# Optimization experiments

Measured on AMD Instinct MI355X. Metric: run time of the kernel, lower is better.

## Reference

```python
import jax, jax.numpy as jnp
import numpy as np

N_NODES = 100000
IN_CH = 256
OUT_CH = 64
N_EDGES = 3200000


def setup_inputs() -> dict:
    key = jax.random.key(0)
    k1, k2, k3, k4 = jax.random.split(key, 4)
    x = jax.random.normal(k1, (N_NODES, IN_CH), dtype=jnp.float32)
    edge_index = jax.random.randint(k2, (2, N_EDGES), 0, N_NODES, dtype=jnp.int64)
    # GCNConv parameters (glorot-style init for W, zeros for bias as in PyG)
    W = jax.random.normal(k3, (IN_CH, OUT_CH), dtype=jnp.float32) / np.sqrt(IN_CH)
    b = jnp.zeros((OUT_CH,), dtype=jnp.float32)
    return {"x": x, "edge_index": edge_index, "W": W, "b": b}


def reference(x, edge_index, W, b):
    N = x.shape[0]
    # --- GCNConv: add self-loops, symmetric degree normalization ---
    loops = jnp.arange(N, dtype=edge_index.dtype)
    src = jnp.concatenate([edge_index[0], loops])  # [E+N]
    dst = jnp.concatenate([edge_index[1], loops])  # [E+N]
    # degree of each target node (edge weights = 1)
    deg = jax.ops.segment_sum(jnp.ones_like(dst, dtype=x.dtype), dst, num_segments=N)
    dinv = jnp.where(deg > 0, jax.lax.rsqrt(deg), 0.0)  # deg^{-1/2}
    norm = dinv[src] * dinv[dst]                        # [E+N]
    # linear transform first (PyG applies lin before propagate)
    h = x @ W                                           # [N, OUT_CH]
    msg = h[src] * norm[:, None]                        # gather + scale
    out = jax.ops.segment_sum(msg, dst, num_segments=N) + b  # scatter-add + bias
    # --- relu + log_softmax ---
    out = jax.nn.relu(out)
    return jax.nn.log_softmax(out, axis=-1)
```

## Files before the change

### kernel.cpp

```cpp
#include <hip/hip_runtime.h>
#include <cstddef>
#include <cstdint>

#define N_NODES 100000
#define IN_CH 256
#define OUT_CH 64
#define N_EDGES 3200000

#define BKT_SHIFT 7
#define BKT_R     128
#define K_BKT     782
#define BKT_CAP   6144
#define T_PART    8192
#define NBLK_PART ((N_EDGES + T_PART - 1) / T_PART)
#define NBLK_GEMM 512
#define N_TILES   (N_NODES / 16)

#define WS_FLAG_OFF   0
#define WS_GCNT_OFF   64
#define WS_DINV_OFF   4096
#define WS_NSE_OFF    404096
#define WS_EDG_OFF    1204224
#define WS_H_OFF      20422656
#define WS_NEED       33222656

#define WSF_DEG_OFF   4096
#define WSF_DINV_OFF  404096
#define WSF_H_OFF     804096

typedef __attribute__((ext_vector_type(8))) short bshort8;
typedef __attribute__((ext_vector_type(4))) float f32x4;
typedef __attribute__((ext_vector_type(2))) float f32x2;
typedef __attribute__((ext_vector_type(4))) unsigned u32x4;

static __device__ __forceinline__ unsigned short f2bf(float f) {
    unsigned u = __builtin_bit_cast(unsigned, f);
    u += 0x7FFFu + ((u >> 16) & 1u);
    return (unsigned short)(u >> 16);
}
static __device__ __forceinline__ float bflo(unsigned u) {
    return __builtin_bit_cast(float, u << 16);
}
static __device__ __forceinline__ float bfhi(unsigned u) {
    return __builtin_bit_cast(float, u & 0xFFFF0000u);
}
static __device__ __forceinline__ f32x2 up2(unsigned u) {
    f32x2 r;
    r.x = __builtin_bit_cast(float, u << 16);
    r.y = __builtin_bit_cast(float, u & 0xFFFF0000u);
    return r;
}

__global__ void probe_kernel(const unsigned* __restrict__ ei, int* __restrict__ flag,
                             unsigned* __restrict__ gcnt) {
    if (blockIdx.x == 0) {
        for (int k = threadIdx.x; k < K_BKT; k += 64) gcnt[k] = 0u;
        if (threadIdx.x == 0) {
            int all0 = 1;
            for (int i = 0; i < 16; ++i) all0 &= (ei[2 * i + 1] == 0u);
            *flag = all0;
        }
    }
}

__device__ __forceinline__ int load_idx(const int* ei32, const long long* ei64,
                                        bool is64, long long pos) {
    return is64 ? (int)ei64[pos] : ei32[pos];
}

static __device__ __forceinline__ void gemm_body(char* smem, int gbid, int nblk,
                                                 const float* __restrict__ x,
                                                 const float* __restrict__ W,
                                                 unsigned short* __restrict__ hs) {
    unsigned short (*Wf)[4][64][8] = (unsigned short (*)[4][64][8])smem;
    const int tid = threadIdx.x;
    const int lane = tid & 63;
    const int wv = tid >> 6;

    for (int i = tid; i < 8 * 4 * 64 * 8; i += 256) {
        int kt = i >> 11;
        int rem = i & 2047;
        int ct = rem >> 9;
        int rem2 = rem & 511;
        int l = rem2 >> 3;
        int j = rem2 & 7;
        int kk = kt * 32 + (l >> 4) * 8 + j;
        int cc = ct * 16 + (l & 15);
        ((unsigned short*)Wf)[i] = f2bf(W[(size_t)kk * OUT_CH + cc]);
    }
    __syncthreads();

    const int r16 = lane & 15;
    const int q = lane >> 4;

    for (int t = gbid * 4 + wv; t < N_TILES; t += nblk * 4) {
        const int row0 = t * 16;
        const float* xrow = &x[(size_t)(row0 + r16) * IN_CH + q * 8];
        f32x4 acc[4] = {{0.f,0.f,0.f,0.f},{0.f,0.f,0.f,0.f},
                        {0.f,0.f,0.f,0.f},{0.f,0.f,0.f,0.f}};
        #pragma unroll
        for (int kt = 0; kt < 8; ++kt) {
            float4 x0 = *(const float4*)&xrow[kt * 32];
            float4 x1 = *(const float4*)&xrow[kt * 32 + 4];
            unsigned p0, p1, p2, p3;
            asm("v_cvt_pk_bf16_f32 %0, %1, %2" : "=v"(p0) : "v"(x0.x), "v"(x0.y));
            asm("v_cvt_pk_bf16_f32 %0, %1, %2" : "=v"(p1) : "v"(x0.z), "v"(x0.w));
            asm("v_cvt_pk_bf16_f32 %0, %1, %2" : "=v"(p2) : "v"(x1.x), "v"(x1.y));
            asm("v_cvt_pk_bf16_f32 %0, %1, %2" : "=v"(p3) : "v"(x1.z), "v"(x1.w));
            u32x4 au = {p0, p1, p2, p3};
            bshort8 af = __builtin_bit_cast(bshort8, au);
            #pragma unroll
            for (int ct = 0; ct < 4; ++ct) {
                bshort8 bf = *(const bshort8*)&Wf[kt][ct][lane][0];
                acc[ct] = __builtin_amdgcn_mfma_f32_16x16x32_bf16(af, bf, acc[ct], 0, 0, 0);
            }
        }
        #pragma unroll
        for (int ct = 0; ct < 4; ++ct) {
            #pragma unroll
            for (int r = 0; r < 4; ++r) {
                int row = row0 + q * 4 + r;
                hs[(size_t)row * OUT_CH + ct * 16 + r16] = f2bf(acc[ct][r]);
            }
        }
    }
}

__global__ __launch_bounds__(512) void partition_kernel(const int* __restrict__ ei32,
                                                        const long long* __restrict__ ei64,
                                                        const int* __restrict__ flag,
                                                        unsigned* __restrict__ gcnt,
                                                        unsigned* __restrict__ edg) {
    __shared__ unsigned hist[K_BKT];
    __shared__ unsigned cur[K_BKT];
    const bool is64 = (*flag != 0);
    const int tid = threadIdx.x;
    const int start = blockIdx.x * T_PART;
    const int end   = min(start + T_PART, N_EDGES);
    const int pbase = start >> 1;
    const int pend  = end >> 1;
    unsigned dcx[8], dcy[8];

    for (int k = tid; k < K_BKT; k += 512) hist[k] = 0u;
    __syncthreads();
    if (is64) {
        const longlong2* d2 = (const longlong2*)&ei64[N_EDGES];
        #pragma unroll
        for (int it = 0; it < 8; ++it) {
            int i = pbase + it * 512 + tid;
            if (i < pend) {
                longlong2 d = d2[i];
                dcx[it] = (unsigned)(int)d.x;
                dcy[it] = (unsigned)(int)d.y;
                atomicAdd(&hist[dcx[it] >> BKT_SHIFT], 1u);
                atomicAdd(&hist[dcy[it] >> BKT_SHIFT], 1u);
            }
        }
    } else {
        const int2* d2 = (const int2*)&ei32[N_EDGES];
        #pragma unroll
        for (int it = 0; it < 8; ++it) {
            int i = pbase + it * 512 + tid;
            if (i < pend) {
                int2 d = d2[i];
                dcx[it] = (unsigned)d.x;
                dcy[it] = (unsigned)d.y;
                atomicAdd(&hist[dcx[it] >> BKT_SHIFT], 1u);
                atomicAdd(&hist[dcy[it] >> BKT_SHIFT], 1u);
            }
        }
    }
    __syncthreads();
    for (int k = tid; k < K_BKT; k += 512) {
        unsigned c = hist[k];
        unsigned base = c ? atomicAdd(&gcnt[k], c) : 0u;
        cur[k] = base + (unsigned)k * BKT_CAP;
    }
    __syncthreads();
    if (is64) {
        const longlong2* s2 = (const longlong2*)&ei64[0];
        #pragma unroll
        for (int it = 0; it < 8; ++it) {
            int i = pbase + it * 512 + tid;
            if (i < pend) {
                longlong2 s = s2[i];
                unsigned dx = dcx[it], dy = dcy[it];
                unsigned p0 = atomicAdd(&cur[dx >> BKT_SHIFT], 1u);
                edg[p0] = (unsigned)s.x | ((dx & (BKT_R - 1)) << 17);
                unsigned p1 = atomicAdd(&cur[dy >> BKT_SHIFT], 1u);
                edg[p1] = (unsigned)s.y | ((dy & (BKT_R - 1)) << 17);
            }
        }
    } else {
        const int2* s2 = (const int2*)&ei32[0];
        #pragma unroll
        for (int it = 0; it < 8; ++it) {
            int i = pbase + it * 512 + tid;
            if (i < pend) {
                int2 s = s2[i];
                unsigned dx = dcx[it], dy = dcy[it];
                unsigned p0 = atomicAdd(&cur[dx >> BKT_SHIFT], 1u);
                edg[p0] = (unsigned)s.x | ((dx & (BKT_R - 1)) << 17);
                unsigned p1 = atomicAdd(&cur[dy >> BKT_SHIFT], 1u);
                edg[p1] = (unsigned)s.y | ((dy & (BKT_R - 1)) << 17);
            }
        }
    }
}

__global__ __launch_bounds__(256) void sortgemm_kernel(unsigned* __restrict__ edg,
                                                       const unsigned* __restrict__ gcnt,
                                                       uint2* __restrict__ nse,
                                                       float* __restrict__ dinv,
                                                       const float* __restrict__ x,
                                                       const float* __restrict__ W,
                                                       unsigned short* __restrict__ hs) {
    __shared__ char smem[32768];
    const int bid = blockIdx.x;
    if (bid < K_BKT) {
        unsigned* ld   = (unsigned*)smem;
        unsigned* hist = (unsigned*)(smem + 24576);
        unsigned* cur  = (unsigned*)(smem + 25088);
        const int k = bid;
        const int t = threadIdx.x;
        const unsigned cnt = min(gcnt[k], (unsigned)BKT_CAP);
        const unsigned base = (unsigned)k * BKT_CAP;

        for (unsigned j = t; j < cnt; j += 256) ld[j] = edg[base + j];
        if (t < BKT_R) hist[t] = 0u;
        __syncthreads();
        for (unsigned j = t; j < cnt; j += 256)
            atomicAdd(&hist[ld[j] >> 17], 1u);
        __syncthreads();
        if (t < BKT_R) cur[t] = hist[t];
        __syncthreads();
        #pragma unroll
        for (int d = 1; d < BKT_R; d <<= 1) {
            unsigned v = (t < BKT_R && t >= d) ? cur[t - d] : 0u;
            __syncthreads();
            if (t < BKT_R) cur[t] += v;
            __syncthreads();
        }
        if (t < BKT_R) {
            unsigned mydeg = hist[t];
            unsigned start = base + cur[t] - mydeg;
            int n = k * BKT_R + t;
            if (n < N_NODES) {
                nse[n] = make_uint2(start, start + mydeg);
                dinv[n] = rsqrtf((float)(mydeg + 1u));
            }
            cur[t] = start;
        }
        __syncthreads();
        for (unsigned j = t; j < cnt; j += 256) {
            unsigned p = ld[j];
            unsigned pos = atomicAdd(&cur[p >> 17], 1u);
            edg[pos] = p & 0x1FFFF;
        }
    } else {
        gemm_body(smem, bid - K_BKT, NBLK_GEMM, x, W, hs);
    }
}

__global__ __launch_bounds__(256) void gemm_only_kernel(const float* __restrict__ x,
                                                        const float* __restrict__ W,
                                                        unsigned short* __restrict__ hs) {
    __shared__ char smem[32768];
    gemm_body(smem, blockIdx.x, gridDim.x, x, W, hs);
}

__global__ __launch_bounds__(256) void reduce_kernel(const unsigned short* __restrict__ hs,
                                                     const float* __restrict__ dinv,
                                                     const uint2* __restrict__ nse,
                                                     const int* __restrict__ ssrc,
                                                     const float* __restrict__ b,
                                                     float* __restrict__ out) {
    const int n = blockIdx.x * 4 + (threadIdx.x >> 6);
    const int lane = threadIdx.x & 63;
    const int q = lane >> 4;
    const int l16 = lane & 15;
    if (n >= N_NODES) return;
    const uint2* h8 = (const uint2*)hs;
    const float dn = dinv[n];
    f32x2 A01 = {0.f, 0.f}, A23 = {0.f, 0.f};
    {
        uint2 sv = h8[(size_t)n * 16 + l16];
        if (q == 0) {
            f32x2 dnv = {dn, dn};
            A01 = up2(sv.x) * dnv;
            A23 = up2(sv.y) * dnv;
        }
    }
    uint2 se = nse[n];
    unsigned j = se.x;
    const unsigned end = se.y;
    for (; j + 32 <= end; j += 32) {
        int s0 = ssrc[j + q];
        int s1 = ssrc[j + 4 + q];
        int s2 = ssrc[j + 8 + q];
        int s3 = ssrc[j + 12 + q];
        int s4 = ssrc[j + 16 + q];
        int s5 = ssrc[j + 20 + q];
        int s6 = ssrc[j + 24 + q];
        int s7 = ssrc[j + 28 + q];
        float f0 = dinv[s0], f1 = dinv[s1], f2 = dinv[s2], f3 = dinv[s3];
        float f4 = dinv[s4], f5 = dinv[s5], f6 = dinv[s6], f7 = dinv[s7];
        uint2 v0 = h8[(size_t)s0 * 16 + l16];
        uint2 v1 = h8[(size_t)s1 * 16 + l16];
        uint2 v2 = h8[(size_t)s2 * 16 + l16];
        uint2 v3 = h8[(size_t)s3 * 16 + l16];
        uint2 v4 = h8[(size_t)s4 * 16 + l16];
        uint2 v5 = h8[(size_t)s5 * 16 + l16];
        uint2 v6 = h8[(size_t)s6 * 16 + l16];
        uint2 v7 = h8[(size_t)s7 * 16 + l16];
        f32x2 F0 = {f0, f0}, F1 = {f1, f1}, F2 = {f2, f2}, F3 = {f3, f3};
        f32x2 F4 = {f4, f4}, F5 = {f5, f5}, F6 = {f6, f6}, F7 = {f7, f7};
        A01 += up2(v0.x) * F0; A23 += up2(v0.y) * F0;
        A01 += up2(v1.x) * F1; A23 += up2(v1.y) * F1;
        A01 += up2(v2.x) * F2; A23 += up2(v2.y) * F2;
        A01 += up2(v3.x) * F3; A23 += up2(v3.y) * F3;
        A01 += up2(v4.x) * F4; A23 += up2(v4.y) * F4;
        A01 += up2(v5.x) * F5; A23 += up2(v5.y) * F5;
        A01 += up2(v6.x) * F6; A23 += up2(v6.y) * F6;
        A01 += up2(v7.x) * F7; A23 += up2(v7.y) * F7;
    }
    for (; j + 16 <= end; j += 16) {
        int s0 = ssrc[j + q];
        int s1 = ssrc[j + 4 + q];
        int s2 = ssrc[j + 8 + q];
        int s3 = ssrc[j + 12 + q];
        float f0 = dinv[s0], f1 = dinv[s1], f2 = dinv[s2], f3 = dinv[s3];
        uint2 v0 = h8[(size_t)s0 * 16 + l16];
        uint2 v1 = h8[(size_t)s1 * 16 + l16];
        uint2 v2 = h8[(size_t)s2 * 16 + l16];
        uint2 v3 = h8[(size_t)s3 * 16 + l16];
        f32x2 F0 = {f0, f0}, F1 = {f1, f1}, F2 = {f2, f2}, F3 = {f3, f3};
        A01 += up2(v0.x) * F0; A23 += up2(v0.y) * F0;
        A01 += up2(v1.x) * F1; A23 += up2(v1.y) * F1;
        A01 += up2(v2.x) * F2; A23 += up2(v2.y) * F2;
        A01 += up2(v3.x) * F3; A23 += up2(v3.y) * F3;
    }
    for (; j + 4 <= end; j += 4) {
        int s = ssrc[j + q];
        float f = dinv[s];
        uint2 v = h8[(size_t)s * 16 + l16];
        f32x2 F = {f, f};
        A01 += up2(v.x) * F; A23 += up2(v.y) * F;
    }
    unsigned rem = end - j;
    if ((unsigned)q < rem) {
        int s = ssrc[j + q];
        float f = dinv[s];
        uint2 v = h8[(size_t)s * 16 + l16];
        f32x2 F = {f, f};
        A01 += up2(v.x) * F; A23 += up2(v.y) * F;
    }
    float a0 = A01.x, a1 = A01.y, a2 = A23.x, a3 = A23.y;
    a0 += __shfl_xor(a0, 16); a0 += __shfl_xor(a0, 32);
    a1 += __shfl_xor(a1, 16); a1 += __shfl_xor(a1, 32);
    a2 += __shfl_xor(a2, 16); a2 += __shfl_xor(a2, 32);
    a3 += __shfl_xor(a3, 16); a3 += __shfl_xor(a3, 32);
    float4 bb = ((const float4*)b)[l16];
    float v0 = fmaxf(fmaf(a0, dn, bb.x), 0.f);
    float v1 = fmaxf(fmaf(a1, dn, bb.y), 0.f);
    float v2 = fmaxf(fmaf(a2, dn, bb.z), 0.f);
    float v3 = fmaxf(fmaf(a3, dn, bb.w), 0.f);
    float m = fmaxf(fmaxf(v0, v1), fmaxf(v2, v3));
    #pragma unroll
    for (int o = 8; o; o >>= 1) m = fmaxf(m, __shfl_xor(m, o));
    float sum = expf(v0 - m) + expf(v1 - m) + expf(v2 - m) + expf(v3 - m);
    #pragma unroll
    for (int o = 8; o; o >>= 1) sum += __shfl_xor(sum, o);
    float ls = logf(sum);
    if (q == 0) {
        float4 r;
        r.x = (v0 - m) - ls; r.y = (v1 - m) - ls;
        r.z = (v2 - m) - ls; r.w = (v3 - m) - ls;
        *(float4*)&out[(size_t)n * OUT_CH + l16 * 4] = r;
    }
}

__global__ __launch_bounds__(256) void deg_kernel(const int* __restrict__ ei32,
                                                  const long long* __restrict__ ei64,
                                                  const int* __restrict__ flag,
                                                  unsigned* __restrict__ deg) {
    const bool is64 = (*flag != 0);
    int i = blockIdx.x * blockDim.x + threadIdx.x;
    const int stride = gridDim.x * blockDim.x;
    for (; i < N_EDGES; i += stride) {
        int d = load_idx(ei32, ei64, is64, (long long)N_EDGES + i);
        atomicAdd(&deg[d], 1u);
    }
}

__global__ __launch_bounds__(256) void dinv_kernel(const unsigned* __restrict__ deg,
                                                   float* __restrict__ dinv) {
    int i = blockIdx.x * blockDim.x + threadIdx.x;
    if (i < N_NODES) dinv[i] = rsqrtf((float)(deg[i] + 1u));
}

__global__ __launch_bounds__(256) void scatter_kernel(const int* __restrict__ ei32,
                                                      const long long* __restrict__ ei64,
                                                      const int* __restrict__ flag,
                                                      const unsigned short* __restrict__ hs,
                                                      const float* __restrict__ dinv,
                                                      float* __restrict__ out) {
    const bool is64 = (*flag != 0);
    const int lane = threadIdx.x & 63;
    int w = blockIdx.x * (blockDim.x >> 6) + (threadIdx.x >> 6);
    const int nw = gridDim.x * (blockDim.x >> 6);
    for (int e = w; e < N_EDGES; e += nw) {
        int s = load_idx(ei32, ei64, is64, e);
        int d = load_idx(ei32, ei64, is64, (long long)N_EDGES + e);
        unsigned short us = hs[(size_t)s * OUT_CH + lane];
        float hv = __builtin_bit_cast(float, (unsigned)us << 16);
        atomicAdd(&out[(size_t)d * OUT_CH + lane], hv * dinv[s] * dinv[d]);
    }
}

__global__ __launch_bounds__(256) void final_kernel(const unsigned short* __restrict__ hs,
                                                    const float* __restrict__ dinv,
                                                    const float* __restrict__ b,
                                                    float* __restrict__ out) {
    const int lane = threadIdx.x & 63;
    int w = blockIdx.x * (blockDim.x >> 6) + (threadIdx.x >> 6);
    const int nw = gridDim.x * (blockDim.x >> 6);
    const float bias = b[lane];
    for (int n = w; n < N_NODES; n += nw) {
        float di = dinv[n];
        unsigned short us = hs[(size_t)n * OUT_CH + lane];
        float hv = __builtin_bit_cast(float, (unsigned)us << 16);
        float v = out[(size_t)n * OUT_CH + lane] + hv * di * di + bias;
        v = fmaxf(v, 0.f);
        float m = v;
        #pragma unroll
        for (int o = 32; o; o >>= 1) m = fmaxf(m, __shfl_xor(m, o));
        float ex = expf(v - m);
        float sum = ex;
        #pragma unroll
        for (int o = 32; o; o >>= 1) sum += __shfl_xor(sum, o);
        out[(size_t)n * OUT_CH + lane] = (v - m) - logf(sum);
    }
}

extern "C" void kernel_launch(void* const* d_in, const int* in_sizes, int n_in,
                              void* d_out, int out_size, void* d_ws, size_t ws_size,
                              hipStream_t stream) {
    const float* x  = (const float*)d_in[0];
    const void*  ei = d_in[1];
    const float* W  = (const float*)d_in[2];
    const float* b  = (const float*)d_in[3];
    float* out = (float*)d_out;

    char* ws = (char*)d_ws;
    int* flag = (int*)(ws + WS_FLAG_OFF);
    unsigned* gcnt = (unsigned*)(ws + WS_GCNT_OFF);

    const int* ei32       = (const int*)ei;
    const long long* ei64 = (const long long*)ei;

    probe_kernel<<<1, 64, 0, stream>>>((const unsigned*)ei, flag, gcnt);

    if (ws_size >= (size_t)WS_NEED) {
        float*    dinv = (float*)(ws + WS_DINV_OFF);
        uint2*    nse  = (uint2*)(ws + WS_NSE_OFF);
        unsigned* edg  = (unsigned*)(ws + WS_EDG_OFF);
        unsigned short* hs = (unsigned short*)(ws + WS_H_OFF);

        partition_kernel<<<NBLK_PART, 512, 0, stream>>>(ei32, ei64, flag, gcnt, edg);
        sortgemm_kernel<<<K_BKT + NBLK_GEMM, 256, 0, stream>>>(
            edg, gcnt, nse, dinv, x, W, hs);
        reduce_kernel<<<(N_NODES + 3) / 4, 256, 0, stream>>>(
            hs, dinv, nse, (const int*)edg, b, out);
    } else {
        unsigned* deg  = (unsigned*)(ws + WSF_DEG_OFF);
        float*    dinv = (float*)(ws + WSF_DINV_OFF);
        unsigned short* hs = (unsigned short*)(ws + WSF_H_OFF);
        hipMemsetAsync(deg, 0, (size_t)N_NODES * sizeof(unsigned), stream);
        hipMemsetAsync(d_out, 0, (size_t)out_size * sizeof(float), stream);
        deg_kernel<<<2048, 256, 0, stream>>>(ei32, ei64, flag, deg);
        dinv_kernel<<<(N_NODES + 255) / 256, 256, 0, stream>>>(deg, dinv);
        gemm_only_kernel<<<NBLK_GEMM, 256, 0, stream>>>(x, W, hs);
        scatter_kernel<<<2048, 256, 0, stream>>>(ei32, ei64, flag, hs, dinv, out);
        final_kernel<<<1024, 256, 0, stream>>>(hs, dinv, b, out);
    }
}
```

Baseline: 161.1 us.

## Stage partitioned edges in LDS and write buckets contiguously to global

New measurement: 157.8 us. -2.0%, faster.

```diff
diff --git a/kernel.cpp b/kernel.cpp
--- a/kernel.cpp
+++ b/kernel.cpp
@@ -131,12 +131,16 @@
                                                         const int* __restrict__ flag,
                                                         unsigned* __restrict__ gcnt,
                                                         unsigned* __restrict__ edg) {
+    __shared__ unsigned ordered[T_PART];
     __shared__ unsigned hist[K_BKT];
+    __shared__ unsigned scan[K_BKT + 1];
     __shared__ unsigned cur[K_BKT];
     const bool is64 = (*flag != 0);
     const int tid = threadIdx.x;
+    const int lane = tid & 63;
     const int start = blockIdx.x * T_PART;
     const int end   = min(start + T_PART, N_EDGES);
+    const int total = end - start;
     const int pbase = start >> 1;
     const int pend  = end >> 1;
     unsigned dcx[8], dcy[8];
@@ -171,10 +175,28 @@
         }
     }
     __syncthreads();
+    if (tid < 64) {
+        if (tid == 0) scan[0] = 0u;
+        unsigned run = 0u;
+        for (int c0 = 0; c0 < K_BKT; c0 += 64) {
+            int k = c0 + lane;
+            unsigned v = (k < K_BKT) ? hist[k] : 0u;
+            unsigned incl = v;
+            #pragma unroll
+            for (int d = 1; d < 64; d <<= 1) {
+                unsigned tq = __shfl_up(incl, d);
+                if (lane >= d) incl += tq;
+            }
+            if (k < K_BKT) scan[k + 1] = run + incl;
+            run += __shfl(incl, 63);
+        }
+    }
+    __syncthreads();
     for (int k = tid; k < K_BKT; k += 512) {
         unsigned c = hist[k];
         unsigned base = c ? atomicAdd(&gcnt[k], c) : 0u;
-        cur[k] = base + (unsigned)k * BKT_CAP;
+        hist[k] = base + (unsigned)k * BKT_CAP;
+        cur[k] = scan[k];
     }
     __syncthreads();
     if (is64) {
@@ -186,9 +208,9 @@
                 longlong2 s = s2[i];
                 unsigned dx = dcx[it], dy = dcy[it];
                 unsigned p0 = atomicAdd(&cur[dx >> BKT_SHIFT], 1u);
-                edg[p0] = (unsigned)s.x | ((dx & (BKT_R - 1)) << 17);
+                ordered[p0] = (unsigned)s.x | ((dx & (BKT_R - 1)) << 17);
                 unsigned p1 = atomicAdd(&cur[dy >> BKT_SHIFT], 1u);
-                edg[p1] = (unsigned)s.y | ((dy & (BKT_R - 1)) << 17);
+                ordered[p1] = (unsigned)s.y | ((dy & (BKT_R - 1)) << 17);
             }
         }
     } else {
@@ -200,11 +222,21 @@
                 int2 s = s2[i];
                 unsigned dx = dcx[it], dy = dcy[it];
                 unsigned p0 = atomicAdd(&cur[dx >> BKT_SHIFT], 1u);
-                edg[p0] = (unsigned)s.x | ((dx & (BKT_R - 1)) << 17);
+                ordered[p0] = (unsigned)s.x | ((dx & (BKT_R - 1)) << 17);
                 unsigned p1 = atomicAdd(&cur[dy >> BKT_SHIFT], 1u);
-                edg[p1] = (unsigned)s.y | ((dy & (BKT_R - 1)) << 17);
-            }
-        }
+                ordered[p1] = (unsigned)s.y | ((dy & (BKT_R - 1)) << 17);
+            }
+        }
+    }
+    __syncthreads();
+    for (int j = tid; j < total; j += 512) {
+        unsigned pr = ordered[j];
+        int lo = 0, hi = K_BKT - 1;
+        while (lo < hi) {
+            int mid = (lo + hi + 1) >> 1;
+            if (scan[mid] <= (unsigned)j) lo = mid; else hi = mid - 1;
+        }
+        edg[hist[lo] + ((unsigned)j - scan[lo])] = pr;
     }
 }
 
```
